# Kernel optimization log

Measured on AMD Instinct MI355X. Metric: run time of the kernel, lower is better.

Reference implementation:

```python
import jax, jax.numpy as jnp
import numpy as np

QW_MAX = 127  # 2**(8-1) - 1


def setup_inputs() -> dict:
    key = jax.random.key(0)
    k1, k2, k3, k4, k5 = jax.random.split(key, 5)
    B, Din, H, Dout = 4096, 1024, 4096, 1024
    x = jax.random.normal(k1, (B, Din), dtype=jnp.float32)
    # float master weights (already transposed, as in quantify_weights: weight.T)
    w1f = jax.random.normal(k2, (Din, H), dtype=jnp.float32) * 0.02
    b1f = jax.random.normal(k3, (H,), dtype=jnp.float32) * 0.02
    w2f = jax.random.normal(k4, (H, Dout), dtype=jnp.float32) * 0.02
    b2f = jax.random.normal(k5, (Dout,), dtype=jnp.float32) * 0.02
    return {"x": x, "w1f": w1f, "b1f": b1f, "w2f": w2f, "b2f": b2f}


def _quantify_pair(w, b):
    # joint max-abs scale over weight and bias (matches quantify(x, x2))
    max_v = jnp.maximum(jnp.max(jnp.abs(w)), jnp.max(jnp.abs(b)))
    scale = max_v / QW_MAX
    wq = jnp.round(w / scale).astype(jnp.int8)
    bq = jnp.round(b / scale).astype(jnp.int8)
    return wq, bq, scale


def _dot_product(q_a, q_b, scale_a, scale_b, target_scale):
    # int8 GEMM with int32 accumulation, then requantize to int16
    y0 = q_a.astype(jnp.int32) @ q_b.astype(jnp.int32)  # [M, N] int32
    scale = scale_a * scale_b / target_scale
    return jnp.round(y0 * scale).astype(jnp.int16)


def reference(x, w1f, b1f, w2f, b2f):
    # weight quantization (done once at init in torch, inlined here)
    w1, b1, s1 = _quantify_pair(w1f, b1f)
    w2, b2, s2 = _quantify_pair(w2f, b2f)
    # dynamic activation quantization
    x_scale = jnp.max(jnp.abs(x)) / QW_MAX
    x_q = jnp.round(x / x_scale).astype(jnp.int8)
    # layer 1: target_scale = s1, so effective multiplier is x_scale
    o1 = _dot_product(x_q, w1, x_scale, s1, s1) + b1.astype(jnp.int16)
    # layer 2: note torch passes scale_1 (not x_scale) here — faithful to source
    o2 = _dot_product(jnp.maximum(o1, 0), w2, s1, s2, s2) + b2.astype(jnp.int16)
    # dequantize
    return o2.astype(jnp.float32) * s2
```

## Files before the change

kernel.cpp:

```cpp
#include <hip/hip_runtime.h>
#include <stdint.h>

typedef int   i32x4 __attribute__((ext_vector_type(4)));
typedef float f32x4 __attribute__((ext_vector_type(4)));

#define WS_PART    0
#define WS_SCALES  6144
#define WS_B1Q     6208
#define WS_B2Q     (6208 + 8192)
#define WS_XQ      32768
#define WS_W1QT    (WS_XQ   + 4096*1024)
#define WS_W2QT    (WS_W1QT + 4096*1024)
#define WS_PS      (WS_W2QT + 4096*1024)
#define WS_PH      (WS_PS   + 4096*4096)

__device__ __forceinline__ void async16(const void* g, void* l) {
  __builtin_amdgcn_global_load_lds(
      (const __attribute__((address_space(1))) unsigned*)g,
      (__attribute__((address_space(3))) unsigned*)l, 16, 0, 0);
}

__global__ void k_absmax3(const float* __restrict__ x, const float* __restrict__ w1,
                          const float* __restrict__ w2, float* __restrict__ part) {
  int seg = blockIdx.x >> 9;
  int b = blockIdx.x & 511;
  const float* p = (seg == 0) ? x : (seg == 1) ? w1 : w2;
  int i = b * 256 + threadIdx.x;
  float m = 0.f;
  #pragma unroll
  for (int it = 0; it < 8; it++) {
    f32x4 v = ((const f32x4*)p)[i + it * 131072];
    m = fmaxf(m, fmaxf(fmaxf(fabsf(v.x), fabsf(v.y)), fmaxf(fabsf(v.z), fabsf(v.w))));
  }
  for (int off = 32; off; off >>= 1) m = fmaxf(m, __shfl_down(m, off));
  __shared__ float red[4];
  if ((threadIdx.x & 63) == 0) red[threadIdx.x >> 6] = m;
  __syncthreads();
  if (threadIdx.x == 0)
    part[blockIdx.x] = fmaxf(fmaxf(red[0], red[1]), fmaxf(red[2], red[3]));
}

__global__ void k_finalize(const float* __restrict__ part, float* __restrict__ scales,
                           const float* __restrict__ b1f, const float* __restrict__ b2f,
                           short* __restrict__ b1q, short* __restrict__ b2q) {
  __shared__ float red[12];
  __shared__ float sh[2];
  int tid = threadIdx.x;
  float mx = 0.f, m1 = 0.f, m2 = 0.f;
  #pragma unroll
  for (int i = 0; i < 2; i++) {
    int j = tid + i * 256;
    mx = fmaxf(mx, part[j]);
    m1 = fmaxf(m1, part[512 + j]);
    m2 = fmaxf(m2, part[1024 + j]);
  }
  for (int i = tid; i < 4096; i += 256) m1 = fmaxf(m1, fabsf(b1f[i]));
  for (int i = tid; i < 1024; i += 256) m2 = fmaxf(m2, fabsf(b2f[i]));
  for (int off = 32; off; off >>= 1) {
    mx = fmaxf(mx, __shfl_down(mx, off));
    m1 = fmaxf(m1, __shfl_down(m1, off));
    m2 = fmaxf(m2, __shfl_down(m2, off));
  }
  if ((tid & 63) == 0) {
    int w = tid >> 6;
    red[w] = mx; red[4 + w] = m1; red[8 + w] = m2;
  }
  __syncthreads();
  if (tid == 0) {
    float MX = fmaxf(fmaxf(red[0], red[1]), fmaxf(red[2], red[3]));
    float M1 = fmaxf(fmaxf(red[4], red[5]), fmaxf(red[6], red[7]));
    float M2 = fmaxf(fmaxf(red[8], red[9]), fmaxf(red[10], red[11]));
    float sx = MX / 127.0f;
    float s1 = M1 / 127.0f;
    float s2 = M2 / 127.0f;
    scales[0] = sx; scales[1] = s1; scales[2] = s2;
    scales[3] = sx * s1 / s1;
    scales[4] = s1 * s2 / s2;
    scales[5] = s2;
    sh[0] = s1; sh[1] = s2;
  }
  __syncthreads();
  float s1 = sh[0], s2 = sh[1];
  for (int i = tid; i < 4096; i += 256) b1q[i] = (short)(int)rintf(b1f[i] / s1);
  for (int i = tid; i < 1024; i += 256) b2q[i] = (short)(int)rintf(b2f[i] / s2);
}

__global__ void k_quant_x(const float* __restrict__ x, const float* __restrict__ scales,
                          i32x4* __restrict__ out) {
  int L = blockIdx.x * 256 + threadIdx.x;
  float s = scales[0];
  int m_in = L & 127, kb = (L >> 7) & 3, tk = (L >> 9) & 15, mblk = L >> 13;
  int m = mblk * 128 + m_in;
  int k0 = (tk * 4 + kb) * 16;
  const f32x4* px = (const f32x4*)(x + m * 1024 + k0);
  int wd[4];
  #pragma unroll
  for (int d = 0; d < 4; d++) {
    f32x4 v = px[d];
    int b0 = (int)rintf(v.x / s) & 255;
    int b1 = (int)rintf(v.y / s) & 255;
    int b2 = (int)rintf(v.z / s) & 255;
    int b3 = (int)rintf(v.w / s) & 255;
    wd[d] = b0 | (b1 << 8) | (b2 << 16) | (b3 << 24);
  }
  i32x4 o; o.x = wd[0]; o.y = wd[1]; o.z = wd[2]; o.w = wd[3];
  out[L] = o;
}

__global__ void k_quantT(const float* __restrict__ w, const float* __restrict__ scales,
                         int sidx, i32x4* __restrict__ out, int C, int tkbits) {
  int L = blockIdx.x * 256 + threadIdx.x;
  float s = scales[sidx];
  int h_in = L & 127;
  int kb = (L >> 7) & 3;
  int tk = (L >> 9) & ((1 << tkbits) - 1);
  int hblk = L >> (9 + tkbits);
  int h = hblk * 128 + h_in;
  int k0 = (tk * 4 + kb) * 16;
  int wd[4];
  #pragma unroll
  for (int d = 0; d < 4; d++) {
    unsigned acc = 0;
    #pragma unroll
    for (int j = 0; j < 4; j++) {
      float v = w[(size_t)(k0 + d * 4 + j) * C + h];
      int q = (int)rintf(v / s) & 255;
      acc |= (unsigned)q << (8 * j);
    }
    wd[d] = (int)acc;
  }
  i32x4 o; o.x = wd[0]; o.y = wd[1]; o.z = wd[2]; o.w = wd[3];
  out[L] = o;
}

__launch_bounds__(256)
__global__ void k_gemm1(const i32x4* __restrict__ Aq, const i32x4* __restrict__ Bq,
                        const float* __restrict__ scales, const short* __restrict__ b1q,
                        unsigned* __restrict__ plane_s, unsigned* __restrict__ plane_h) {
  __shared__ i32x4 As[2][512];
  __shared__ i32x4 Bs[2][512];
  int tid = threadIdx.x;
  int bb = blockIdx.x;
  int hb = blockIdx.y;
  int lane = tid & 63, wid = tid >> 6;
  int wm = wid & 1, wn = wid >> 1;
  int g = lane >> 4, l15 = lane & 15;

  i32x4 acc[4][4];
  #pragma unroll
  for (int r = 0; r < 4; r++)
    #pragma unroll
    for (int c = 0; c < 4; c++) acc[r][c] = (i32x4)(0);

  int abase = g * 128 + wm * 64 + l15;
  int bbase = g * 128 + wn * 64 + l15;

  const i32x4* gA = Aq + (size_t)hb * 16 * 512;
  const i32x4* gB = Bq + (size_t)bb * 16 * 512;

  async16(gA + tid, &As[0][tid]);
  async16(gA + tid + 256, &As[0][tid + 256]);
  async16(gB + tid, &Bs[0][tid]);
  async16(gB + tid + 256, &Bs[0][tid + 256]);

  for (int t = 0; t < 16; ++t) {
    int cur = t & 1;
    __syncthreads();
    if (t + 1 < 16) {
      const i32x4* ga = gA + (t + 1) * 512;
      const i32x4* gb = gB + (t + 1) * 512;
      async16(ga + tid, &As[cur ^ 1][tid]);
      async16(ga + tid + 256, &As[cur ^ 1][tid + 256]);
      async16(gb + tid, &Bs[cur ^ 1][tid]);
      async16(gb + tid + 256, &Bs[cur ^ 1][tid + 256]);
    }
    i32x4 af[4], bf[4];
    #pragma unroll
    for (int r = 0; r < 4; r++) af[r] = As[cur][abase + r * 16];
    #pragma unroll
    for (int c = 0; c < 4; c++) bf[c] = Bs[cur][bbase + c * 16];
    #pragma unroll
    for (int r = 0; r < 4; r++)
      #pragma unroll
      for (int c = 0; c < 4; c++)
        acc[r][c] = __builtin_amdgcn_mfma_i32_16x16x64_i8(af[r], bf[c], acc[r][c], 0, 0, 0);
  }

  float mult1 = scales[3];
  int t2base = hb * 2 + wm;
  #pragma unroll
  for (int r = 0; r < 4; r++) {
    int hbase = hb * 128 + wm * 64 + r * 16 + 4 * g;
    const short* bp = b1q + hbase;
    short bq0 = bp[0], bq1 = bp[1], bq2 = bp[2], bq3 = bp[3];
    #pragma unroll
    for (int c = 0; c < 4; c++) {
      unsigned lo = 0, hi = 0;
      #pragma unroll
      for (int q = 0; q < 4; q++) {
        int y0 = acc[r][c][q];
        short bqv = (q == 0) ? bq0 : (q == 1) ? bq1 : (q == 2) ? bq2 : bq3;
        int o = (short)((int)rintf((float)y0 * mult1) + (int)bqv);
        int a = o > 0 ? o : 0;
        int s8 = (int)(signed char)(a & 0xFF);
        int h8 = (a >> 8) + (s8 < 0 ? 1 : 0);
        lo |= (unsigned)(s8 & 0xFF) << (8 * q);
        hi |= (unsigned)(h8 & 0xFF) << (8 * q);
      }
      int m_in = wn * 64 + c * 16 + l15;
      unsigned idx = (((unsigned)(bb * 64 + t2base) * 512u + (unsigned)(r * 128 + m_in)) << 2) + g;
      plane_s[idx] = lo;
      plane_h[idx] = hi;
    }
  }
}

__launch_bounds__(256)
__global__ void k_gemm2(const i32x4* __restrict__ Ps, const i32x4* __restrict__ Ph,
                        const i32x4* __restrict__ Bq, const float* __restrict__ scales,
                        const short* __restrict__ b2q, float* __restrict__ out) {
  __shared__ i32x4 AsS[2][256];
  __shared__ i32x4 AsH[2][256];
  __shared__ i32x4 Bs[2][512];
  int tid = threadIdx.x;
  int L = blockIdx.x;
  int mb = L & 63;
  int nb = L >> 6;
  int mblk = mb >> 1, half = mb & 1;
  int lane = tid & 63, wid = tid >> 6;
  int wm = wid & 1, wn = wid >> 1;
  int g = lane >> 4, l15 = lane & 15;

  i32x4 accS[2][4], accH[2][4];
  #pragma unroll
  for (int r = 0; r < 2; r++)
    #pragma unroll
    for (int c = 0; c < 4; c++) { accS[r][c] = (i32x4)(0); accH[r][c] = (i32x4)(0); }

  int aoff = wid * 128 + half * 64 + lane;
  int abase = g * 64 + wm * 32 + l15;
  int bbase = g * 128 + wn * 64 + l15;

  const i32x4* gS = Ps + (size_t)mblk * 64 * 512;
  const i32x4* gH = Ph + (size_t)mblk * 64 * 512;
  const i32x4* gB = Bq + (size_t)nb * 64 * 512;

  async16(gS + aoff, &AsS[0][tid]);
  async16(gH + aoff, &AsH[0][tid]);
  async16(gB + tid, &Bs[0][tid]);
  async16(gB + tid + 256, &Bs[0][tid + 256]);

  for (int t = 0; t < 64; ++t) {
    int cur = t & 1;
    __syncthreads();
    if (t + 1 < 64) {
      const i32x4* gs = gS + (t + 1) * 512;
      const i32x4* gh = gH + (t + 1) * 512;
      const i32x4* gb = gB + (t + 1) * 512;
      async16(gs + aoff, &AsS[cur ^ 1][tid]);
      async16(gh + aoff, &AsH[cur ^ 1][tid]);
      async16(gb + tid, &Bs[cur ^ 1][tid]);
      async16(gb + tid + 256, &Bs[cur ^ 1][tid + 256]);
    }
    i32x4 aS[2], aH[2], bf[4];
    #pragma unroll
    for (int r = 0; r < 2; r++) {
      aS[r] = AsS[cur][abase + r * 16];
      aH[r] = AsH[cur][abase + r * 16];
    }
    #pragma unroll
    for (int c = 0; c < 4; c++) bf[c] = Bs[cur][bbase + c * 16];
    #pragma unroll
    for (int r = 0; r < 2; r++)
      #pragma unroll
      for (int c = 0; c < 4; c++) {
        accS[r][c] = __builtin_amdgcn_mfma_i32_16x16x64_i8(aS[r], bf[c], accS[r][c], 0, 0, 0);
        accH[r][c] = __builtin_amdgcn_mfma_i32_16x16x64_i8(aH[r], bf[c], accH[r][c], 0, 0, 0);
      }
  }

  float mult2 = scales[4];
  float s2 = scales[5];
  #pragma unroll
  for (int r = 0; r < 2; r++) {
    int m0 = mb * 64 + wm * 32 + r * 16 + 4 * g;
    #pragma unroll
    for (int c = 0; c < 4; c++) {
      int n = nb * 128 + wn * 64 + c * 16 + l15;
      int bqv = (int)b2q[n];
      #pragma unroll
      for (int q = 0; q < 4; q++) {
        int y0 = accS[r][c][q] + accH[r][c][q] * 256;
        int o = (short)((int)rintf((float)y0 * mult2) + bqv);
        out[(size_t)(m0 + q) * 1024 + n] = (float)o * s2;
      }
    }
  }
}

extern "C" void kernel_launch(void* const* d_in, const int* in_sizes, int n_in,
                              void* d_out, int out_size, void* d_ws, size_t ws_size,
                              hipStream_t stream) {
  const float* x   = (const float*)d_in[0];
  const float* w1f = (const float*)d_in[1];
  const float* b1f = (const float*)d_in[2];
  const float* w2f = (const float*)d_in[3];
  const float* b2f = (const float*)d_in[4];
  float* out = (float*)d_out;

  char* ws = (char*)d_ws;
  float*  part    = (float*)(ws + WS_PART);
  float*  scales  = (float*)(ws + WS_SCALES);
  short*  b1q     = (short*)(ws + WS_B1Q);
  short*  b2q     = (short*)(ws + WS_B2Q);
  i32x4*  xq      = (i32x4*)(ws + WS_XQ);
  i32x4*  w1qt    = (i32x4*)(ws + WS_W1QT);
  i32x4*  w2qt    = (i32x4*)(ws + WS_W2QT);
  unsigned* ps    = (unsigned*)(ws + WS_PS);
  unsigned* ph    = (unsigned*)(ws + WS_PH);

  k_absmax3<<<1536, 256, 0, stream>>>(x, w1f, w2f, part);
  k_finalize<<<1, 256, 0, stream>>>(part, scales, b1f, b2f, b1q, b2q);
  k_quant_x<<<1024, 256, 0, stream>>>(x, scales, xq);
  k_quantT<<<1024, 256, 0, stream>>>(w1f, scales, 1, w1qt, 4096, 4);
  k_quantT<<<1024, 256, 0, stream>>>(w2f, scales, 2, w2qt, 1024, 6);
  k_gemm1<<<dim3(32, 32), 256, 0, stream>>>(w1qt, xq, scales, b1q, ps, ph);
  k_gemm2<<<512, 256, 0, stream>>>((const i32x4*)ps, (const i32x4*)ph, w2qt,
                                   scales, b2q, out);
}
```

Before: 196.7 us.

## Fuse scale finalize into consumers, merge quant kernels, split-K gemm2 across 512 threads

Removes the single-block finalize kernel and recomputes the scale reductions redundantly inside each consumer block, merges the three quantization kernels into one launch, and folds bias quantization into the GEMM prologues. gemm2 now uses 512 threads with a two-way split-K whose partial sums are merged through LDS, and its block index is swizzled. The aim is fewer launches and serial single-block work plus more parallelism in gemm2. In exchange every block repeats small reductions over the partial-max buffer and the bias vectors, and gemm2 uses more LDS and adds an extra merge step.

```diff
diff --git a/kernel.cpp b/kernel.cpp
--- a/kernel.cpp
+++ b/kernel.cpp
@@ -5,9 +5,6 @@
 typedef float f32x4 __attribute__((ext_vector_type(4)));
 
 #define WS_PART    0
-#define WS_SCALES  6144
-#define WS_B1Q     6208
-#define WS_B2Q     (6208 + 8192)
 #define WS_XQ      32768
 #define WS_W1QT    (WS_XQ   + 4096*1024)
 #define WS_W2QT    (WS_W1QT + 4096*1024)
@@ -18,6 +15,26 @@
   __builtin_amdgcn_global_load_lds(
       (const __attribute__((address_space(1))) unsigned*)g,
       (__attribute__((address_space(3))) unsigned*)l, 16, 0, 0);
+}
+
+__device__ __forceinline__ float block_absmax(const float* __restrict__ p0, int n0,
+                                              const float* __restrict__ p1, int n1,
+                                              float* red, float* slot) {
+  int tid = threadIdx.x, nt = blockDim.x;
+  float m = 0.f;
+  for (int i = tid; i < n0; i += nt) m = fmaxf(m, fabsf(p0[i]));
+  if (p1) for (int i = tid; i < n1; i += nt) m = fmaxf(m, fabsf(p1[i]));
+  for (int off = 32; off; off >>= 1) m = fmaxf(m, __shfl_down(m, off));
+  if ((tid & 63) == 0) red[tid >> 6] = m;
+  __syncthreads();
+  if (tid == 0) {
+    int nw = nt >> 6;
+    float M = red[0];
+    for (int w = 1; w < nw; w++) M = fmaxf(M, red[w]);
+    *slot = M;
+  }
+  __syncthreads();
+  return *slot;
 }
 
 __global__ void k_absmax3(const float* __restrict__ x, const float* __restrict__ w1,
@@ -40,77 +57,10 @@
     part[blockIdx.x] = fmaxf(fmaxf(red[0], red[1]), fmaxf(red[2], red[3]));
 }
 
-__global__ void k_finalize(const float* __restrict__ part, float* __restrict__ scales,
-                           const float* __restrict__ b1f, const float* __restrict__ b2f,
-                           short* __restrict__ b1q, short* __restrict__ b2q) {
-  __shared__ float red[12];
-  __shared__ float sh[2];
-  int tid = threadIdx.x;
-  float mx = 0.f, m1 = 0.f, m2 = 0.f;
-  #pragma unroll
-  for (int i = 0; i < 2; i++) {
-    int j = tid + i * 256;
-    mx = fmaxf(mx, part[j]);
-    m1 = fmaxf(m1, part[512 + j]);
-    m2 = fmaxf(m2, part[1024 + j]);
-  }
-  for (int i = tid; i < 4096; i += 256) m1 = fmaxf(m1, fabsf(b1f[i]));
-  for (int i = tid; i < 1024; i += 256) m2 = fmaxf(m2, fabsf(b2f[i]));
-  for (int off = 32; off; off >>= 1) {
-    mx = fmaxf(mx, __shfl_down(mx, off));
-    m1 = fmaxf(m1, __shfl_down(m1, off));
-    m2 = fmaxf(m2, __shfl_down(m2, off));
-  }
-  if ((tid & 63) == 0) {
-    int w = tid >> 6;
-    red[w] = mx; red[4 + w] = m1; red[8 + w] = m2;
-  }
-  __syncthreads();
-  if (tid == 0) {
-    float MX = fmaxf(fmaxf(red[0], red[1]), fmaxf(red[2], red[3]));
-    float M1 = fmaxf(fmaxf(red[4], red[5]), fmaxf(red[6], red[7]));
-    float M2 = fmaxf(fmaxf(red[8], red[9]), fmaxf(red[10], red[11]));
-    float sx = MX / 127.0f;
-    float s1 = M1 / 127.0f;
-    float s2 = M2 / 127.0f;
-    scales[0] = sx; scales[1] = s1; scales[2] = s2;
-    scales[3] = sx * s1 / s1;
-    scales[4] = s1 * s2 / s2;
-    scales[5] = s2;
-    sh[0] = s1; sh[1] = s2;
-  }
-  __syncthreads();
-  float s1 = sh[0], s2 = sh[1];
-  for (int i = tid; i < 4096; i += 256) b1q[i] = (short)(int)rintf(b1f[i] / s1);
-  for (int i = tid; i < 1024; i += 256) b2q[i] = (short)(int)rintf(b2f[i] / s2);
-}
-
-__global__ void k_quant_x(const float* __restrict__ x, const float* __restrict__ scales,
-                          i32x4* __restrict__ out) {
-  int L = blockIdx.x * 256 + threadIdx.x;
-  float s = scales[0];
-  int m_in = L & 127, kb = (L >> 7) & 3, tk = (L >> 9) & 15, mblk = L >> 13;
-  int m = mblk * 128 + m_in;
-  int k0 = (tk * 4 + kb) * 16;
-  const f32x4* px = (const f32x4*)(x + m * 1024 + k0);
-  int wd[4];
-  #pragma unroll
-  for (int d = 0; d < 4; d++) {
-    f32x4 v = px[d];
-    int b0 = (int)rintf(v.x / s) & 255;
-    int b1 = (int)rintf(v.y / s) & 255;
-    int b2 = (int)rintf(v.z / s) & 255;
-    int b3 = (int)rintf(v.w / s) & 255;
-    wd[d] = b0 | (b1 << 8) | (b2 << 16) | (b3 << 24);
-  }
-  i32x4 o; o.x = wd[0]; o.y = wd[1]; o.z = wd[2]; o.w = wd[3];
-  out[L] = o;
-}
-
-__global__ void k_quantT(const float* __restrict__ w, const float* __restrict__ scales,
-                         int sidx, i32x4* __restrict__ out, int C, int tkbits) {
-  int L = blockIdx.x * 256 + threadIdx.x;
-  float s = scales[sidx];
+__device__ __forceinline__ void quantT_body(const float* __restrict__ w, float s,
+                                            i32x4* __restrict__ out, int C, int tkbits,
+                                            int b) {
+  int L = b * 256 + threadIdx.x;
   int h_in = L & 127;
   int kb = (L >> 7) & 3;
   int tk = (L >> 9) & ((1 << tkbits) - 1);
@@ -133,12 +83,52 @@
   out[L] = o;
 }
 
+__global__ void k_prep(const float* __restrict__ x, const float* __restrict__ w1f,
+                       const float* __restrict__ w2f, const float* __restrict__ b1f,
+                       const float* __restrict__ b2f, const float* __restrict__ part,
+                       i32x4* __restrict__ xq, i32x4* __restrict__ w1qt,
+                       i32x4* __restrict__ w2qt) {
+  __shared__ float red[4];
+  __shared__ float slot;
+  int seg = blockIdx.x >> 10;
+  int b = blockIdx.x & 1023;
+  if (seg == 0) {
+    float s = block_absmax(part, 512, nullptr, 0, red, &slot) / 127.0f;
+    int L = b * 256 + threadIdx.x;
+    int m_in = L & 127, kb = (L >> 7) & 3, tk = (L >> 9) & 15, mblk = L >> 13;
+    int m = mblk * 128 + m_in;
+    int k0 = (tk * 4 + kb) * 16;
+    const f32x4* px = (const f32x4*)(x + m * 1024 + k0);
+    int wd[4];
+    #pragma unroll
+    for (int d = 0; d < 4; d++) {
+      f32x4 v = px[d];
+      int b0 = (int)rintf(v.x / s) & 255;
+      int b1 = (int)rintf(v.y / s) & 255;
+      int b2 = (int)rintf(v.z / s) & 255;
+      int b3 = (int)rintf(v.w / s) & 255;
+      wd[d] = b0 | (b1 << 8) | (b2 << 16) | (b3 << 24);
+    }
+    i32x4 o; o.x = wd[0]; o.y = wd[1]; o.z = wd[2]; o.w = wd[3];
+    xq[L] = o;
+  } else if (seg == 1) {
+    float s = block_absmax(part + 512, 512, b1f, 4096, red, &slot) / 127.0f;
+    quantT_body(w1f, s, w1qt, 4096, 4, b);
+  } else {
+    float s = block_absmax(part + 1024, 512, b2f, 1024, red, &slot) / 127.0f;
+    quantT_body(w2f, s, w2qt, 1024, 6, b);
+  }
+}
+
 __launch_bounds__(256)
 __global__ void k_gemm1(const i32x4* __restrict__ Aq, const i32x4* __restrict__ Bq,
-                        const float* __restrict__ scales, const short* __restrict__ b1q,
+                        const float* __restrict__ part, const float* __restrict__ b1f,
                         unsigned* __restrict__ plane_s, unsigned* __restrict__ plane_h) {
   __shared__ i32x4 As[2][512];
   __shared__ i32x4 Bs[2][512];
+  __shared__ float red[4];
+  __shared__ float slot;
+  __shared__ int b1s[128];
   int tid = threadIdx.x;
   int bb = blockIdx.x;
   int hb = blockIdx.y;
@@ -146,15 +136,6 @@
   int wm = wid & 1, wn = wid >> 1;
   int g = lane >> 4, l15 = lane & 15;
 
-  i32x4 acc[4][4];
-  #pragma unroll
-  for (int r = 0; r < 4; r++)
-    #pragma unroll
-    for (int c = 0; c < 4; c++) acc[r][c] = (i32x4)(0);
-
-  int abase = g * 128 + wm * 64 + l15;
-  int bbase = g * 128 + wn * 64 + l15;
-
   const i32x4* gA = Aq + (size_t)hb * 16 * 512;
   const i32x4* gB = Bq + (size_t)bb * 16 * 512;
 
@@ -162,6 +143,21 @@
   async16(gA + tid + 256, &As[0][tid + 256]);
   async16(gB + tid, &Bs[0][tid]);
   async16(gB + tid + 256, &Bs[0][tid + 256]);
+
+  float sx  = block_absmax(part, 512, nullptr, 0, red, &slot) / 127.0f;
+  float s1v = block_absmax(part + 512, 512, b1f, 4096, red, &slot) / 127.0f;
+  float mult1 = sx * s1v / s1v;
+  for (int i = tid; i < 128; i += 256)
+    b1s[i] = (int)rintf(b1f[hb * 128 + i] / s1v);
+
+  i32x4 acc[4][4];
+  #pragma unroll
+  for (int r = 0; r < 4; r++)
+    #pragma unroll
+    for (int c = 0; c < 4; c++) acc[r][c] = (i32x4)(0);
+
+  int abase = g * 128 + wm * 64 + l15;
+  int bbase = g * 128 + wn * 64 + l15;
 
   for (int t = 0; t < 16; ++t) {
     int cur = t & 1;
@@ -186,21 +182,19 @@
         acc[r][c] = __builtin_amdgcn_mfma_i32_16x16x64_i8(af[r], bf[c], acc[r][c], 0, 0, 0);
   }
 
-  float mult1 = scales[3];
   int t2base = hb * 2 + wm;
   #pragma unroll
   for (int r = 0; r < 4; r++) {
-    int hbase = hb * 128 + wm * 64 + r * 16 + 4 * g;
-    const short* bp = b1q + hbase;
-    short bq0 = bp[0], bq1 = bp[1], bq2 = bp[2], bq3 = bp[3];
+    int hloc = wm * 64 + r * 16 + 4 * g;
+    int bq0 = b1s[hloc], bq1 = b1s[hloc + 1], bq2 = b1s[hloc + 2], bq3 = b1s[hloc + 3];
     #pragma unroll
     for (int c = 0; c < 4; c++) {
       unsigned lo = 0, hi = 0;
       #pragma unroll
       for (int q = 0; q < 4; q++) {
         int y0 = acc[r][c][q];
-        short bqv = (q == 0) ? bq0 : (q == 1) ? bq1 : (q == 2) ? bq2 : bq3;
-        int o = (short)((int)rintf((float)y0 * mult1) + (int)bqv);
+        int bqv = (q == 0) ? bq0 : (q == 1) ? bq1 : (q == 2) ? bq2 : bq3;
+        int o = (short)((int)rintf((float)y0 * mult1) + bqv);
         int a = o > 0 ? o : 0;
         int s8 = (int)(signed char)(a & 0xFF);
         int h8 = (a >> 8) + (s8 < 0 ? 1 : 0);
@@ -215,21 +209,46 @@
   }
 }
 
-__launch_bounds__(256)
+__launch_bounds__(512)
 __global__ void k_gemm2(const i32x4* __restrict__ Ps, const i32x4* __restrict__ Ph,
-                        const i32x4* __restrict__ Bq, const float* __restrict__ scales,
-                        const short* __restrict__ b2q, float* __restrict__ out) {
-  __shared__ i32x4 AsS[2][256];
-  __shared__ i32x4 AsH[2][256];
-  __shared__ i32x4 Bs[2][512];
+                        const i32x4* __restrict__ Bq, const float* __restrict__ part,
+                        const float* __restrict__ b1f, const float* __restrict__ b2f,
+                        float* __restrict__ out) {
+  __shared__ i32x4 st[4096];
+  float* red  = (float*)&st[1024];
+  float* slot = red + 8;
+
   int tid = threadIdx.x;
   int L = blockIdx.x;
-  int mb = L & 63;
+  int mb = ((L & 7) << 3) | ((L >> 3) & 7);
   int nb = L >> 6;
   int mblk = mb >> 1, half = mb & 1;
-  int lane = tid & 63, wid = tid >> 6;
-  int wm = wid & 1, wn = wid >> 1;
+  int wid = tid >> 6, lane = tid & 63;
+  int kh = wid >> 2, w2 = wid & 3;
+  int wm = w2 & 1, wn = w2 >> 1;
   int g = lane >> 4, l15 = lane & 15;
+  int t256 = tid & 255;
+  int sbase = kh * 2048;
+  int a_idx = (t256 >> 6) * 128 + half * 64 + (t256 & 63);
+
+  {
+    int t = kh * 32;
+    const i32x4* pS = Ps + ((size_t)(mblk * 64 + t) << 9);
+    const i32x4* pH = Ph + ((size_t)(mblk * 64 + t) << 9);
+    const i32x4* pB = Bq + ((size_t)(nb * 64 + t) << 9);
+    async16(pS + a_idx, &st[sbase + t256]);
+    async16(pH + a_idx, &st[sbase + 256 + t256]);
+    async16(pB + t256, &st[sbase + 512 + t256]);
+    async16(pB + t256 + 256, &st[sbase + 768 + t256]);
+  }
+
+  float s1v = block_absmax(part + 512, 512, b1f, 4096, red, slot) / 127.0f;
+  float s2v = block_absmax(part + 1024, 512, b2f, 1024, red, slot) / 127.0f;
+  float mult2 = s1v * s2v / s2v;
+  int bq[4];
+  #pragma unroll
+  for (int c = 0; c < 4; c++)
+    bq[c] = (int)rintf(b2f[nb * 128 + wn * 64 + c * 16 + l15] / s2v);
 
   i32x4 accS[2][4], accH[2][4];
   #pragma unroll
@@ -237,39 +256,29 @@
     #pragma unroll
     for (int c = 0; c < 4; c++) { accS[r][c] = (i32x4)(0); accH[r][c] = (i32x4)(0); }
 
-  int aoff = wid * 128 + half * 64 + lane;
-  int abase = g * 64 + wm * 32 + l15;
-  int bbase = g * 128 + wn * 64 + l15;
-
-  const i32x4* gS = Ps + (size_t)mblk * 64 * 512;
-  const i32x4* gH = Ph + (size_t)mblk * 64 * 512;
-  const i32x4* gB = Bq + (size_t)nb * 64 * 512;
-
-  async16(gS + aoff, &AsS[0][tid]);
-  async16(gH + aoff, &AsH[0][tid]);
-  async16(gB + tid, &Bs[0][tid]);
-  async16(gB + tid + 256, &Bs[0][tid + 256]);
-
-  for (int t = 0; t < 64; ++t) {
-    int cur = t & 1;
+  for (int tt = 0; tt < 32; ++tt) {
+    int cur = tt & 1;
     __syncthreads();
-    if (t + 1 < 64) {
-      const i32x4* gs = gS + (t + 1) * 512;
-      const i32x4* gh = gH + (t + 1) * 512;
-      const i32x4* gb = gB + (t + 1) * 512;
-      async16(gs + aoff, &AsS[cur ^ 1][tid]);
-      async16(gh + aoff, &AsH[cur ^ 1][tid]);
-      async16(gb + tid, &Bs[cur ^ 1][tid]);
-      async16(gb + tid + 256, &Bs[cur ^ 1][tid + 256]);
-    }
+    if (tt + 1 < 32) {
+      int t = kh * 32 + tt + 1;
+      const i32x4* pS = Ps + ((size_t)(mblk * 64 + t) << 9);
+      const i32x4* pH = Ph + ((size_t)(mblk * 64 + t) << 9);
+      const i32x4* pB = Bq + ((size_t)(nb * 64 + t) << 9);
+      int R1 = sbase + (cur ^ 1) * 1024;
+      async16(pS + a_idx, &st[R1 + t256]);
+      async16(pH + a_idx, &st[R1 + 256 + t256]);
+      async16(pB + t256, &st[R1 + 512 + t256]);
+      async16(pB + t256 + 256, &st[R1 + 768 + t256]);
+    }
+    int R = sbase + cur * 1024;
     i32x4 aS[2], aH[2], bf[4];
     #pragma unroll
     for (int r = 0; r < 2; r++) {
-      aS[r] = AsS[cur][abase + r * 16];
-      aH[r] = AsH[cur][abase + r * 16];
-    }
-    #pragma unroll
-    for (int c = 0; c < 4; c++) bf[c] = Bs[cur][bbase + c * 16];
+      aS[r] = st[R + g * 64 + wm * 32 + r * 16 + l15];
+      aH[r] = st[R + 256 + g * 64 + wm * 32 + r * 16 + l15];
+    }
+    #pragma unroll
+    for (int c = 0; c < 4; c++) bf[c] = st[R + 512 + g * 128 + wn * 64 + c * 16 + l15];
     #pragma unroll
     for (int r = 0; r < 2; r++)
       #pragma unroll
@@ -279,20 +288,40 @@
       }
   }
 
-  float mult2 = scales[4];
-  float s2 = scales[5];
-  #pragma unroll
-  for (int r = 0; r < 2; r++) {
-    int m0 = mb * 64 + wm * 32 + r * 16 + 4 * g;
-    #pragma unroll
-    for (int c = 0; c < 4; c++) {
-      int n = nb * 128 + wn * 64 + c * 16 + l15;
-      int bqv = (int)b2q[n];
-      #pragma unroll
-      for (int q = 0; q < 4; q++) {
-        int y0 = accS[r][c][q] + accH[r][c][q] * 256;
-        int o = (short)((int)rintf((float)y0 * mult2) + bqv);
-        out[(size_t)(m0 + q) * 1024 + n] = (float)o * s2;
+  int y0p[2][4][4];
+  #pragma unroll
+  for (int r = 0; r < 2; r++)
+    #pragma unroll
+    for (int c = 0; c < 4; c++)
+      #pragma unroll
+      for (int q = 0; q < 4; q++)
+        y0p[r][c][q] = accS[r][c][q] + accH[r][c][q] * 256;
+
+  __syncthreads();
+  int* mg = (int*)st;
+  if (kh == 1) {
+    #pragma unroll
+    for (int r = 0; r < 2; r++)
+      #pragma unroll
+      for (int c = 0; c < 4; c++)
+        #pragma unroll
+        for (int q = 0; q < 4; q++)
+          mg[((r * 4 + c) * 4 + q) * 256 + t256] = y0p[r][c][q];
+  }
+  __syncthreads();
+  if (kh == 0) {
+    #pragma unroll
+    for (int r = 0; r < 2; r++) {
+      int m0 = mb * 64 + wm * 32 + r * 16 + 4 * g;
+      #pragma unroll
+      for (int c = 0; c < 4; c++) {
+        int n = nb * 128 + wn * 64 + c * 16 + l15;
+        #pragma unroll
+        for (int q = 0; q < 4; q++) {
+          int y0 = y0p[r][c][q] + mg[((r * 4 + c) * 4 + q) * 256 + t256];
+          int o = (short)((int)rintf((float)y0 * mult2) + bq[c]);
+          out[(size_t)(m0 + q) * 1024 + n] = (float)o * s2v;
+        }
       }
     }
   }
@@ -310,9 +339,6 @@
 
   char* ws = (char*)d_ws;
   float*  part    = (float*)(ws + WS_PART);
-  float*  scales  = (float*)(ws + WS_SCALES);
-  short*  b1q     = (short*)(ws + WS_B1Q);
-  short*  b2q     = (short*)(ws + WS_B2Q);
   i32x4*  xq      = (i32x4*)(ws + WS_XQ);
   i32x4*  w1qt    = (i32x4*)(ws + WS_W1QT);
   i32x4*  w2qt    = (i32x4*)(ws + WS_W2QT);
@@ -320,11 +346,8 @@
   unsigned* ph    = (unsigned*)(ws + WS_PH);
 
   k_absmax3<<<1536, 256, 0, stream>>>(x, w1f, w2f, part);
-  k_finalize<<<1, 256, 0, stream>>>(part, scales, b1f, b2f, b1q, b2q);
-  k_quant_x<<<1024, 256, 0, stream>>>(x, scales, xq);
-  k_quantT<<<1024, 256, 0, stream>>>(w1f, scales, 1, w1qt, 4096, 4);
-  k_quantT<<<1024, 256, 0, stream>>>(w2f, scales, 2, w2qt, 1024, 6);
-  k_gemm1<<<dim3(32, 32), 256, 0, stream>>>(w1qt, xq, scales, b1q, ps, ph);
-  k_gemm2<<<512, 256, 0, stream>>>((const i32x4*)ps, (const i32x4*)ph, w2qt,
-                                   scales, b2q, out);
-}
+  k_prep<<<3072, 256, 0, stream>>>(x, w1f, w2f, b1f, b2f, part, xq, w1qt, w2qt);
+  k_gemm1<<<dim3(32, 32), 256, 0, stream>>>(w1qt, xq, part, b1f, ps, ph);
+  k_gemm2<<<512, 512, 0, stream>>>((const i32x4*)ps, (const i32x4*)ph, w2qt,
+                                   part, b1f, b2f, out);
+}
```

Result: faster. 178.3 us (-9.3%).
